# Performance work log

Measured on AMD Instinct MI355X. Metric: run time of the kernel, lower is better.

The kernel has to match this reference:

```python
import jax, jax.numpy as jnp
import numpy as np

LMAX = 3                               # self.lmax = lmax_arg(2) + 1
L2 = LMAX * LMAX                       # 9 = 1 + 3 + 5
N_MLP = 2
DEG_IDX = np.repeat(np.arange(LMAX), 2 * np.arange(LMAX) + 1)   # [9] block -> degree index
SEG = np.zeros((LMAX, L2), np.float32)                          # one-hot segment matrix [3,9]
SEG[DEG_IDX, np.arange(L2)] = 1.0


def setup_inputs() -> dict:
    key = jax.random.key(0)
    ks = jax.random.split(key, 8)
    B, M, F, K = 8, 1024, 64, 64
    x = jax.random.normal(ks[0], (B, M, F, L2), jnp.float32)
    y = jax.random.normal(ks[1], (B, M, F, L2), jnp.float32)
    # Glorot-ish scales so tanh stays in its active range
    s0 = 1.0 / np.sqrt(F * F * LMAX)
    sh = 1.0 / np.sqrt(K)
    wx0 = jax.random.normal(ks[2], (K, F, F, LMAX), jnp.float32) * s0
    wy0 = jax.random.normal(ks[3], (K, F, F, LMAX), jnp.float32) * s0
    wx_h = jax.random.normal(ks[4], (N_MLP, K, K), jnp.float32) * sh
    wy_h = jax.random.normal(ks[5], (N_MLP, K, K), jnp.float32) * sh
    wxf = jax.random.normal(ks[6], (LMAX, F, K), jnp.float32) * sh
    wyf = jax.random.normal(ks[7], (LMAX, F, K), jnp.float32) * sh
    return {"x": x, "y": y, "wx0": wx0, "wy0": wy0,
            "wx_h": wx_h, "wy_h": wy_h, "wxf": wxf, "wyf": wyf}


def reference(x, y, wx0, wy0, wx_h, wy_h, wxf, wyf):
    seg = jnp.asarray(SEG)                                   # [lmax, l2]
    # cross-product gate from the l=1 (vector) components
    x1 = x[..., 1:4]                                         # [B,M,F,3]
    y1 = y[..., 1:4]
    gate = jnp.sum(jnp.cross(x1, y1) * y[..., 0:3], axis=-1) # [B,M,F]
    xg = x * gate[..., None]                                 # gated x, [B,M,F,l2]
    # outer product over features + contiguous segment-sum over degree blocks
    # mix[b,m,f,g,l] = sum_{s in block l} xg[b,m,g,s] * y[b,m,f,s]
    mix = jnp.einsum('bmgs,bmfs,ls->bmfgl', xg, y, seg)      # [B,M,F,F,lmax]
    mix_x = jnp.einsum('bmfgl,kfgl->bmk', mix, wx0)          # [B,M,k]
    mix_y = jnp.einsum('bmfgl,kfgl->bmk', mix, wy0)
    for i in range(N_MLP):
        mix_x = jnp.tanh(mix_x @ wx_h[i])
        mix_y = jnp.tanh(mix_y @ wy_h[i])
    mix_x = jnp.tanh(jnp.einsum('bmk,lfk->bmfl', mix_x, wxf))  # [B,M,F,lmax]
    mix_y = jnp.tanh(jnp.einsum('bmk,lfk->bmfl', mix_y, wyf))
    # broadcast each degree back over its 2l+1 components (gather == tf.repeat)
    res = mix_x[..., DEG_IDX] * xg + mix_y[..., DEG_IDX] * y   # [B,M,F,l2]
    return res
```

## Files before the change

### kernel.cpp

```cpp
#include <hip/hip_runtime.h>
#include <hip/hip_bf16.h>

typedef __attribute__((ext_vector_type(8))) short short8;
typedef __attribute__((ext_vector_type(16))) float f32x16;
typedef __fp16 h2 __attribute__((ext_vector_type(2)));
typedef unsigned short ushort_t;

#define DEVFN static __device__ __forceinline__
#define MFMA32 __builtin_amdgcn_mfma_f32_32x32x16_bf16

DEVFN float bf2f(unsigned short u){
  union { unsigned int i; float f; } v; v.i = ((unsigned int)u) << 16; return v.f;
}
DEVFN unsigned short f2bf(float f){
  unsigned int u = __float_as_uint(f);
  unsigned int r = u + 0x7FFFu + ((u >> 16) & 1u);
  return (unsigned short)(r >> 16);
}
DEVFN unsigned int pkbf(float lo, float hi){
  __hip_bfloat162 h = __float22bfloat162_rn(make_float2(lo, hi));
  return *reinterpret_cast<unsigned int*>(&h);
}
DEVFN h2 pkrtz(float a, float b){ return __builtin_amdgcn_cvt_pkrtz(a, b); }
DEVFN h2 u2h(unsigned int u){ union { unsigned int u; h2 h; } v; v.u = u; return v.h; }
#if __has_builtin(__builtin_amdgcn_fdot2)
DEVFN float fdot2(h2 a, h2 b, float c){ return __builtin_amdgcn_fdot2(a, b, c, false); }
#else
DEVFN float fdot2(h2 a, h2 b, float c){ return c + (float)a[0]*(float)b[0] + (float)a[1]*(float)b[1]; }
#endif
DEVFN float tanh_fast(float x){
  float t = __builtin_amdgcn_exp2f(x * 2.885390081777926815f);
  return 1.0f - 2.0f * __builtin_amdgcn_rcpf(t + 1.0f);
}
DEVFN int kmap(int h, int j){ return 4*h + (j & 3) + 8*(j >> 2); }

__global__ void bake_w0(const float* __restrict__ wx0, const float* __restrict__ wy0,
                        ushort_t* __restrict__ wfrag){
  int slot = blockIdx.x * 256 + threadIdx.x;
  int lane = slot & 63;
  int q = slot >> 6;
  int blk = q % 6; int q2 = q / 6;
  int l = blk >> 1, nt = blk & 1;
  int nh = q2 & 1; int gq = (q2 >> 1) & 3; int f = q2 >> 3;
  int h = lane >> 5;
  int k = nt*32 + (lane & 31);
  const float* w = nh ? wy0 : wx0;
  unsigned int pk[4];
#pragma unroll
  for (int jj = 0; jj < 4; ++jj){
    int g0 = gq*16 + kmap(h, 2*jj);
    int g1 = gq*16 + kmap(h, 2*jj + 1);
    unsigned int b0 = f2bf(w[((k*64 + f)*64 + g0)*3 + l]);
    unsigned int b1 = f2bf(w[((k*64 + f)*64 + g1)*3 + l]);
    pk[jj] = b0 | (b1 << 16);
  }
  *reinterpret_cast<uint4*>(wfrag + (size_t)slot * 8) = make_uint4(pk[0], pk[1], pk[2], pk[3]);
}

__global__ void bake_wh(const float* __restrict__ wxh, const float* __restrict__ wyh,
                        ushort_t* __restrict__ whfrag){
  int slot = blockIdx.x * 256 + threadIdx.x;
  int lane = slot & 63;
  int q = slot >> 6;
  int nt = q & 1; q >>= 1;
  int c  = q & 3; q >>= 2;
  int path = q & 1; int layer = q >> 1;
  const float* w = path ? wyh : wxh;
  int n = nt*32 + (lane & 31);
  int h = lane >> 5;
  unsigned int pk[4];
#pragma unroll
  for (int jj = 0; jj < 4; ++jj){
    int k0 = c*16 + kmap(h, 2*jj);
    int k1 = c*16 + kmap(h, 2*jj + 1);
    unsigned int b0 = f2bf(w[layer*4096 + k0*64 + n]);
    unsigned int b1 = f2bf(w[layer*4096 + k1*64 + n]);
    pk[jj] = b0 | (b1 << 16);
  }
  *reinterpret_cast<uint4*>(whfrag + (size_t)slot * 8) = make_uint4(pk[0], pk[1], pk[2], pk[3]);
}

__global__ void bake_wf(const float* __restrict__ wxf, const float* __restrict__ wyf,
                        ushort_t* __restrict__ wffrag){
  int slot = blockIdx.x * 256 + threadIdx.x;
  int lane = slot & 63;
  int q = slot >> 6;
  int ntf = q % 6;
  int q2 = q / 6;
  int c = q2 & 3; int path = q2 >> 2;
  const float* w = path ? wyf : wxf;
  int n = ntf*32 + (lane & 31);
  int lw = n >> 6, fw = n & 63;
  int h = lane >> 5;
  unsigned int pk[4];
#pragma unroll
  for (int jj = 0; jj < 4; ++jj){
    int k0 = c*16 + kmap(h, 2*jj);
    int k1 = c*16 + kmap(h, 2*jj + 1);
    unsigned int b0 = f2bf(w[(lw*64 + fw)*64 + k0]);
    unsigned int b1 = f2bf(w[(lw*64 + fw)*64 + k1]);
    pk[jj] = b0 | (b1 << 16);
  }
  *reinterpret_cast<uint4*>(wffrag + (size_t)slot * 8) = make_uint4(pk[0], pk[1], pk[2], pk[3]);
}

struct BSet { uint4 b[6]; };
union U4 { uint4 u; short8 s; };

__global__ __launch_bounds__(256)
void gemm9(const float* __restrict__ x, const float* __restrict__ y,
           const ushort_t* __restrict__ wfrag, float* __restrict__ mix){
  extern __shared__ char lds[];
  unsigned int* YHd = (unsigned int*)lds;
  ushort_t* YHh = (ushort_t*)lds;
  float* Xf = (float*)(lds + 41600);
  float (*red)[64][33] = (float (*)[64][33])(lds + 41600);

  const int bid = blockIdx.x;
  const int id = (bid & 7)*64 + (bid >> 3);
  const int nh = id & 1, mb = id >> 1;
  const int pbase = mb * 32;

  const int t = threadIdx.x, lane = t & 63, gq = t >> 6;
  const int h = lane >> 5, pr = lane & 31;

  const float* xb = x + (size_t)pbase * 576;
  const float* yb = y + (size_t)pbase * 576;

#pragma unroll
  for (int c = 0; c < 18; ++c){
    int q = t + c*256;
    int p = q / 144, off = (q - p*144) * 4;
    float4 v = *(const float4*)(yb + p*576 + off);
#pragma unroll
    for (int i = 0; i < 4; ++i){
      int flat = off + i;
      int f = flat / 9, s = flat - f*9;
      float vv = (i==0) ? v.x : (i==1) ? v.y : (i==2) ? v.z : v.w;
      union { __fp16 hf; ushort_t u; } cv; cv.hf = (__fp16)vv;
      YHh[p*650 + f*10 + s] = cv.u;
    }
  }
#pragma unroll
  for (int c = 0; c < 9; ++c){
    int q = t + c*256;
    int p = q / 72, off = (q - p*72) * 4;
    float4 v = *(const float4*)(xb + p*576 + off);
    float* dst = Xf + p*290 + off;
    dst[0] = v.x; dst[1] = v.y; dst[2] = v.z; dst[3] = v.w;
  }
  __syncthreads();

  h2 xg[8][5];
  auto compute_xg = [&](int hf){
#pragma unroll
    for (int j = 0; j < 8; ++j){
      int gl = (gq & 1)*16 + kmap(h, j);
      int gg = hf*32 + gl;
      const float* xp = Xf + pr*290 + gl*9;
      unsigned int yd0 = YHd[pr*325 + gg*5 + 0];
      unsigned int yd1 = YHd[pr*325 + gg*5 + 1];
      h2 y01 = u2h(yd0), y23v = u2h(yd1);
      float y0 = (float)y01[0], y1 = (float)y01[1];
      float y2 = (float)y23v[0], y3 = (float)y23v[1];
      float x1 = xp[1], x2 = xp[2], x3 = xp[3];
      float gate = (x2*y3 - x3*y2)*y0 + (x3*y1 - x1*y3)*y1 + (x1*y2 - x2*y1)*y2;
      xg[j][0] = pkrtz(xp[0]*gate, x1*gate);
      xg[j][1] = pkrtz(x2*gate, x3*gate);
      xg[j][2] = pkrtz(xp[4]*gate, xp[5]*gate);
      xg[j][3] = pkrtz(xp[6]*gate, xp[7]*gate);
      xg[j][4] = pkrtz(xp[8]*gate, 0.f);
    }
  };
  if (gq < 2) compute_xg(0);
  __syncthreads();
#pragma unroll
  for (int c = 0; c < 9; ++c){
    int q = t + c*256;
    int p = q / 72, off = (q - p*72) * 4;
    float4 v = *(const float4*)(xb + p*576 + 288 + off);
    float* dst = Xf + p*290 + off;
    dst[0] = v.x; dst[1] = v.y; dst[2] = v.z; dst[3] = v.w;
  }
  __syncthreads();
  if (gq >= 2) compute_xg(1);
  __syncthreads();

  f32x16 acc0, acc1;
#pragma unroll
  for (int e = 0; e < 16; ++e){ acc0[e] = 0.f; acc1[e] = 0.f; }

  const ushort_t* wt = wfrag + (size_t)(gq*2 + nh)*3072 + (size_t)lane*8;
  const unsigned int* yrow = YHd + pr*325;

  auto ldB = [&](int f, BSet& B){
    const ushort_t* p0 = wt + (size_t)f * 24576;
#pragma unroll
    for (int i = 0; i < 6; ++i) B.b[i] = *reinterpret_cast<const uint4*>(p0 + i*512);
  };
  auto ldYh = [&](int f, unsigned int* Yr){
#pragma unroll
    for (int d = 0; d < 5; ++d) Yr[d] = yrow[f*5 + d];
  };
  auto agen_mfma = [&](const unsigned int* Yr, const BSet& B){
    h2 y0m = u2h(Yr[0] & 0xFFFFu);
    h2 y1m = u2h(Yr[0] & 0xFFFF0000u);
    h2 y23 = u2h(Yr[1]), y45 = u2h(Yr[2]), y67 = u2h(Yr[3]);
    h2 y8p = u2h(Yr[4] & 0xFFFFu);
    float a0[8], a1[8], a2[8];
#pragma unroll
    for (int j = 0; j < 8; ++j){
      a0[j] = fdot2(xg[j][0], y0m, 0.f);
      a1[j] = fdot2(xg[j][1], y23, fdot2(xg[j][0], y1m, 0.f));
      a2[j] = fdot2(xg[j][4], y8p, fdot2(xg[j][3], y67, fdot2(xg[j][2], y45, 0.f)));
    }
    U4 fA0, fA1, fA2;
    fA0.u = make_uint4(pkbf(a0[0],a0[1]), pkbf(a0[2],a0[3]), pkbf(a0[4],a0[5]), pkbf(a0[6],a0[7]));
    fA1.u = make_uint4(pkbf(a1[0],a1[1]), pkbf(a1[2],a1[3]), pkbf(a1[4],a1[5]), pkbf(a1[6],a1[7]));
    fA2.u = make_uint4(pkbf(a2[0],a2[1]), pkbf(a2[2],a2[3]), pkbf(a2[4],a2[5]), pkbf(a2[6],a2[7]));
    U4 b0, b1, b2, b3, b4, b5;
    b0.u = B.b[0]; b1.u = B.b[1]; b2.u = B.b[2];
    b3.u = B.b[3]; b4.u = B.b[4]; b5.u = B.b[5];
    acc0 = MFMA32(fA0.s, b0.s, acc0, 0, 0, 0);
    acc1 = MFMA32(fA0.s, b1.s, acc1, 0, 0, 0);
    acc0 = MFMA32(fA1.s, b2.s, acc0, 0, 0, 0);
    acc1 = MFMA32(fA1.s, b3.s, acc1, 0, 0, 0);
    acc0 = MFMA32(fA2.s, b4.s, acc0, 0, 0, 0);
    acc1 = MFMA32(fA2.s, b5.s, acc1, 0, 0, 0);
  };

  BSet Ba, Bb;
  unsigned int Ya[5], Yb[5];
  ldB(0, Ba); ldYh(0, Ya);
  ldB(1, Bb); ldYh(1, Yb);

#pragma unroll 1
  for (int s = 0; s < 64; s += 2){
    agen_mfma(Ya, Ba);
    const int s2 = (s + 2 < 64) ? s + 2 : 63;
    ldB(s2, Ba); ldYh(s2, Ya);
    agen_mfma(Yb, Bb);
    const int s3 = (s + 3 < 64) ? s + 3 : 63;
    ldB(s3, Bb); ldYh(s3, Yb);
  }

  __syncthreads();
  if (gq >= 2){
#pragma unroll
    for (int e = 0; e < 16; ++e){
      red[gq-2][lane][e]      = acc0[e];
      red[gq-2][lane][16 + e] = acc1[e];
    }
  }
  __syncthreads();
  if (gq < 2){
#pragma unroll
    for (int e = 0; e < 16; ++e){
      acc0[e] += red[gq][lane][e];
      acc1[e] += red[gq][lane][16 + e];
    }
  }
  __syncthreads();
  if (gq == 1){
#pragma unroll
    for (int e = 0; e < 16; ++e){
      red[0][lane][e]      = acc0[e];
      red[0][lane][16 + e] = acc1[e];
    }
  }
  __syncthreads();
  if (gq == 0){
#pragma unroll
    for (int e = 0; e < 16; ++e){
      float v0 = acc0[e] + red[0][lane][e];
      float v1 = acc1[e] + red[0][lane][16 + e];
      int rowm = (e & 3) + 8*(e >> 2) + 4*h;
      float* d = mix + (size_t)(pbase + rowm)*128 + nh*64 + pr;
      d[0]  = v0;
      d[32] = v1;
    }
  }
}

__global__ __launch_bounds__(256, 1)
void mlp_final(const float* __restrict__ x, const float* __restrict__ y,
               const ushort_t* __restrict__ whfrag,
               const ushort_t* __restrict__ wffrag,
               const float* __restrict__ mix, float* __restrict__ out){
  extern __shared__ char ldsm[];
  ushort_t* hw = (ushort_t*)ldsm;
  const int t = threadIdx.x;
  const long pbase = (long)blockIdx.x * 32;

  {
    int p = t >> 3, n0 = (t & 7) * 16;
    const float* src = mix + (pbase + p)*128 + n0;
    int path = n0 >> 6, nn = n0 & 63;
    ushort_t* dst = hw + (path*2)*2176 + p*68 + nn;
#pragma unroll
    for (int q2 = 0; q2 < 16; ++q2) dst[q2] = f2bf(src[q2]);
  }
  __syncthreads();

  const int w = t >> 6, lane = t & 63;
  const int path = w >> 1, ntw = w & 1;
  const int prow = lane & 31, h = lane >> 5;
  int cur = 0;

#pragma unroll
  for (int layer = 0; layer < 2; ++layer){
    const ushort_t* act = hw + (path*2 + cur)*2176;
    f32x16 acc;
#pragma unroll
    for (int r = 0; r < 16; ++r) acc[r] = 0.f;
#pragma unroll
    for (int c = 0; c < 4; ++c){
      int ab = prow*68 + c*16 + 4*h;
      ushort4 lo = *(const ushort4*)&act[ab];
      ushort4 hi = *(const ushort4*)&act[ab + 8];
      short8 av; av[0]=lo.x; av[1]=lo.y; av[2]=lo.z; av[3]=lo.w;
      av[4]=hi.x; av[5]=hi.y; av[6]=hi.z; av[7]=hi.w;
      short8 bv = *(const short8*)(whfrag + ((((layer*2 + path)*4 + c)*2 + ntw)*512 + lane*8));
      acc = MFMA32(av, bv, acc, 0, 0, 0);
    }
    ushort_t* nact = hw + (path*2 + (cur ^ 1))*2176;
#pragma unroll
    for (int r = 0; r < 16; ++r){
      int p = (r & 3) + 8*(r >> 2) + 4*h;
      nact[p*68 + ntw*32 + prow] = f2bf(tanh_fast(acc[r]));
    }
    cur ^= 1;
    __syncthreads();
  }

  {
    const ushort_t* act = hw + (path*2 + cur)*2176;
    ushort_t* ob = hw + 8704 + path*6272;
#pragma unroll
    for (int e = 0; e < 3; ++e){
      int ntf = ntw*3 + e;
      f32x16 acc;
#pragma unroll
      for (int r = 0; r < 16; ++r) acc[r] = 0.f;
#pragma unroll
      for (int c = 0; c < 4; ++c){
        int ab = prow*68 + c*16 + 4*h;
        ushort4 lo = *(const ushort4*)&act[ab];
        ushort4 hi = *(const ushort4*)&act[ab + 8];
        short8 av; av[0]=lo.x; av[1]=lo.y; av[2]=lo.z; av[3]=lo.w;
        av[4]=hi.x; av[5]=hi.y; av[6]=hi.z; av[7]=hi.w;
        short8 bv = *(const short8*)(wffrag + (((path*4 + c)*6 + ntf)*512 + lane*8));
        acc = MFMA32(av, bv, acc, 0, 0, 0);
      }
#pragma unroll
      for (int r = 0; r < 16; ++r){
        int p = (r & 3) + 8*(r >> 2) + 4*h;
        ob[p*196 + ntf*32 + prow] = f2bf(tanh_fast(acc[r]));
      }
    }
  }
  __syncthreads();

  const ushort_t* oxb = hw + 8704;
  const ushort_t* oyb = hw + 8704 + 6272;
#pragma unroll 1
  for (int rep = 0; rep < 8; ++rep){
    int idx = t + rep*256;
    int p = idx >> 6, fq = idx & 63;
    const float* xr = x + ((pbase + p)*64 + fq)*9;
    const float* yr = y + ((pbase + p)*64 + fq)*9;
    float xv[9], yv[9];
#pragma unroll
    for (int s = 0; s < 9; ++s){ xv[s] = xr[s]; yv[s] = yr[s]; }
    float c0 = xv[2]*yv[3] - xv[3]*yv[2];
    float c1 = xv[3]*yv[1] - xv[1]*yv[3];
    float c2 = xv[1]*yv[2] - xv[2]*yv[1];
    float gate = c0*yv[0] + c1*yv[1] + c2*yv[2];
    float ox0 = bf2f(oxb[p*196 + fq]);
    float ox1 = bf2f(oxb[p*196 + 64 + fq]);
    float ox2 = bf2f(oxb[p*196 + 128 + fq]);
    float oy0 = bf2f(oyb[p*196 + fq]);
    float oy1 = bf2f(oyb[p*196 + 64 + fq]);
    float oy2 = bf2f(oyb[p*196 + 128 + fq]);
    float* orow = out + ((pbase + p)*64 + fq)*9;
    orow[0] = ox0*xv[0]*gate + oy0*yv[0];
#pragma unroll
    for (int s = 1; s < 4; ++s) orow[s] = ox1*xv[s]*gate + oy1*yv[s];
#pragma unroll
    for (int s = 4; s < 9; ++s) orow[s] = ox2*xv[s]*gate + oy2*yv[s];
  }
}

extern "C" void kernel_launch(void* const* d_in, const int* in_sizes, int n_in,
                              void* d_out, int out_size, void* d_ws, size_t ws_size,
                              hipStream_t stream){
  (void)in_sizes; (void)n_in; (void)out_size; (void)ws_size;
  const float* x   = (const float*)d_in[0];
  const float* y   = (const float*)d_in[1];
  const float* wx0 = (const float*)d_in[2];
  const float* wy0 = (const float*)d_in[3];
  const float* wxh = (const float*)d_in[4];
  const float* wyh = (const float*)d_in[5];
  const float* wxf = (const float*)d_in[6];
  const float* wyf = (const float*)d_in[7];
  float* out = (float*)d_out;
  char* ws = (char*)d_ws;
  ushort_t* wfrag  = (ushort_t*)(ws);
  ushort_t* whfrag = (ushort_t*)(ws + 3145728);
  ushort_t* wffrag = (ushort_t*)(ws + 3178496);
  float* mix       = (float*)(ws + 3227648);

  (void)hipFuncSetAttribute((const void*)gemm9,
        hipFuncAttributeMaxDynamicSharedMemorySize, 78720);
  (void)hipFuncSetAttribute((const void*)mlp_final,
        hipFuncAttributeMaxDynamicSharedMemorySize, 43520);

  hipLaunchKernelGGL(bake_w0, dim3(768), dim3(256), 0, stream, wx0, wy0, wfrag);
  hipLaunchKernelGGL(bake_wh, dim3(8),   dim3(256), 0, stream, wxh, wyh, whfrag);
  hipLaunchKernelGGL(bake_wf, dim3(12),  dim3(256), 0, stream, wxf, wyf, wffrag);
  hipLaunchKernelGGL(gemm9,   dim3(512), dim3(256), 78720, stream, x, y, wfrag, mix);
  hipLaunchKernelGGL(mlp_final, dim3(256), dim3(256), 42496, stream, x, y, whfrag, wffrag, mix, out);
}
```

Baseline: 91.70 us.

## Read x directly from global in gemm, shrink LDS, coalesce w0 bake reads

The gemm kernel stops staging x in shared memory. Each warp now computes its gated-x fragments straight from global memory, with no two-phase staged compute. The cross-warp reduction becomes a serial 3-step accumulate into one small buffer, which cuts LDS from about 78KB to about 50KB per block so more blocks can be resident. The w0 bake kernel is rewritten to read weights contiguously (one thread per weight triple) and scatter 2-byte writes, and pkbf now uses an inline bf16 pack instruction. The cost is uncoalesced strided global reads of x and extra barriers in the reduction.

```diff
diff --git a/kernel.cpp b/kernel.cpp
--- a/kernel.cpp
+++ b/kernel.cpp
@@ -17,9 +17,10 @@
   unsigned int r = u + 0x7FFFu + ((u >> 16) & 1u);
   return (unsigned short)(r >> 16);
 }
-DEVFN unsigned int pkbf(float lo, float hi){
-  __hip_bfloat162 h = __float22bfloat162_rn(make_float2(lo, hi));
-  return *reinterpret_cast<unsigned int*>(&h);
+DEVFN unsigned int pkbf(float a, float b){
+  unsigned int r;
+  asm("v_cvt_pk_bf16_f32 %0, %1, %2" : "=v"(r) : "v"(a), "v"(b));
+  return r;
 }
 DEVFN h2 pkrtz(float a, float b){ return __builtin_amdgcn_cvt_pkrtz(a, b); }
 DEVFN h2 u2h(unsigned int u){ union { unsigned int u; h2 h; } v; v.u = u; return v.h; }
@@ -36,25 +37,22 @@
 
 __global__ void bake_w0(const float* __restrict__ wx0, const float* __restrict__ wy0,
                         ushort_t* __restrict__ wfrag){
-  int slot = blockIdx.x * 256 + threadIdx.x;
-  int lane = slot & 63;
-  int q = slot >> 6;
-  int blk = q % 6; int q2 = q / 6;
-  int l = blk >> 1, nt = blk & 1;
-  int nh = q2 & 1; int gq = (q2 >> 1) & 3; int f = q2 >> 3;
-  int h = lane >> 5;
-  int k = nt*32 + (lane & 31);
-  const float* w = nh ? wy0 : wx0;
-  unsigned int pk[4];
-#pragma unroll
-  for (int jj = 0; jj < 4; ++jj){
-    int g0 = gq*16 + kmap(h, 2*jj);
-    int g1 = gq*16 + kmap(h, 2*jj + 1);
-    unsigned int b0 = f2bf(w[((k*64 + f)*64 + g0)*3 + l]);
-    unsigned int b1 = f2bf(w[((k*64 + f)*64 + g1)*3 + l]);
-    pk[jj] = b0 | (b1 << 16);
-  }
-  *reinterpret_cast<uint4*>(wfrag + (size_t)slot * 8) = make_uint4(pk[0], pk[1], pk[2], pk[3]);
+  int idx = blockIdx.x * 256 + threadIdx.x;
+  int g = idx & 63; int r = idx >> 6;
+  int f = r & 63; r >>= 6;
+  int k = r & 63; int path = r >> 6;
+  const float* w = path ? wy0 : wx0;
+  const float* src = w + ((size_t)(k*64 + f)*64 + g)*3;
+  float v0 = src[0], v1 = src[1], v2 = src[2];
+  int gq = g >> 4, gl = g & 15;
+  int h = (gl >> 2) & 1;
+  int j = (gl & 3) | ((gl >> 3) << 2);
+  int lane = h*32 + (k & 31);
+  int nt = k >> 5;
+  size_t base = (size_t)((f*4 + gq)*2 + path)*3072 + (size_t)lane*8 + j;
+  wfrag[base + 0*512 + (size_t)nt*512] = f2bf(v0);
+  wfrag[base + 2*512 + (size_t)nt*512] = f2bf(v1);
+  wfrag[base + 4*512 + (size_t)nt*512] = f2bf(v2);
 }
 
 __global__ void bake_wh(const float* __restrict__ wxh, const float* __restrict__ wyh,
@@ -108,13 +106,12 @@
 union U4 { uint4 u; short8 s; };
 
 __global__ __launch_bounds__(256)
-void gemm9(const float* __restrict__ x, const float* __restrict__ y,
-           const ushort_t* __restrict__ wfrag, float* __restrict__ mix){
+void gemm10(const float* __restrict__ x, const float* __restrict__ y,
+            const ushort_t* __restrict__ wfrag, float* __restrict__ mix){
   extern __shared__ char lds[];
   unsigned int* YHd = (unsigned int*)lds;
   ushort_t* YHh = (ushort_t*)lds;
-  float* Xf = (float*)(lds + 41600);
-  float (*red)[64][33] = (float (*)[64][33])(lds + 41600);
+  float (*red)[33] = (float (*)[33])(lds + 41600);
 
   const int bid = blockIdx.x;
   const int id = (bid & 7)*64 + (bid >> 3);
@@ -124,7 +121,6 @@
   const int t = threadIdx.x, lane = t & 63, gq = t >> 6;
   const int h = lane >> 5, pr = lane & 31;
 
-  const float* xb = x + (size_t)pbase * 576;
   const float* yb = y + (size_t)pbase * 576;
 
 #pragma unroll
@@ -141,50 +137,26 @@
       YHh[p*650 + f*10 + s] = cv.u;
     }
   }
-#pragma unroll
-  for (int c = 0; c < 9; ++c){
-    int q = t + c*256;
-    int p = q / 72, off = (q - p*72) * 4;
-    float4 v = *(const float4*)(xb + p*576 + off);
-    float* dst = Xf + p*290 + off;
-    dst[0] = v.x; dst[1] = v.y; dst[2] = v.z; dst[3] = v.w;
-  }
   __syncthreads();
 
   h2 xg[8][5];
-  auto compute_xg = [&](int hf){
-#pragma unroll
-    for (int j = 0; j < 8; ++j){
-      int gl = (gq & 1)*16 + kmap(h, j);
-      int gg = hf*32 + gl;
-      const float* xp = Xf + pr*290 + gl*9;
-      unsigned int yd0 = YHd[pr*325 + gg*5 + 0];
-      unsigned int yd1 = YHd[pr*325 + gg*5 + 1];
-      h2 y01 = u2h(yd0), y23v = u2h(yd1);
-      float y0 = (float)y01[0], y1 = (float)y01[1];
-      float y2 = (float)y23v[0], y3 = (float)y23v[1];
-      float x1 = xp[1], x2 = xp[2], x3 = xp[3];
-      float gate = (x2*y3 - x3*y2)*y0 + (x3*y1 - x1*y3)*y1 + (x1*y2 - x2*y1)*y2;
-      xg[j][0] = pkrtz(xp[0]*gate, x1*gate);
-      xg[j][1] = pkrtz(x2*gate, x3*gate);
-      xg[j][2] = pkrtz(xp[4]*gate, xp[5]*gate);
-      xg[j][3] = pkrtz(xp[6]*gate, xp[7]*gate);
-      xg[j][4] = pkrtz(xp[8]*gate, 0.f);
-    }
-  };
-  if (gq < 2) compute_xg(0);
-  __syncthreads();
-#pragma unroll
-  for (int c = 0; c < 9; ++c){
-    int q = t + c*256;
-    int p = q / 72, off = (q - p*72) * 4;
-    float4 v = *(const float4*)(xb + p*576 + 288 + off);
-    float* dst = Xf + p*290 + off;
-    dst[0] = v.x; dst[1] = v.y; dst[2] = v.z; dst[3] = v.w;
-  }
-  __syncthreads();
-  if (gq >= 2) compute_xg(1);
-  __syncthreads();
+#pragma unroll
+  for (int j = 0; j < 8; ++j){
+    const int g = gq*16 + kmap(h, j);
+    const float* xp = x + (size_t)(pbase + pr)*576 + g*9;
+    unsigned int yd0 = YHd[pr*325 + g*5 + 0];
+    unsigned int yd1 = YHd[pr*325 + g*5 + 1];
+    h2 y01 = u2h(yd0), y23v = u2h(yd1);
+    float y0 = (float)y01[0], y1 = (float)y01[1];
+    float y2 = (float)y23v[0], y3 = (float)y23v[1];
+    float x1 = xp[1], x2 = xp[2], x3 = xp[3];
+    float gate = (x2*y3 - x3*y2)*y0 + (x3*y1 - x1*y3)*y1 + (x1*y2 - x2*y1)*y2;
+    xg[j][0] = pkrtz(xp[0]*gate, x1*gate);
+    xg[j][1] = pkrtz(x2*gate, x3*gate);
+    xg[j][2] = pkrtz(xp[4]*gate, xp[5]*gate);
+    xg[j][3] = pkrtz(xp[6]*gate, xp[7]*gate);
+    xg[j][4] = pkrtz(xp[8]*gate, 0.f);
+  }
 
   f32x16 acc0, acc1;
 #pragma unroll
@@ -245,39 +217,32 @@
   }
 
   __syncthreads();
-  if (gq >= 2){
+#pragma unroll 1
+  for (int rr = 1; rr <= 3; ++rr){
+    if (gq == rr){
+#pragma unroll
+      for (int e = 0; e < 16; ++e){
+        red[lane][e]      = acc0[e];
+        red[lane][16 + e] = acc1[e];
+      }
+    }
+    __syncthreads();
+    if (gq == 0){
+#pragma unroll
+      for (int e = 0; e < 16; ++e){
+        acc0[e] += red[lane][e];
+        acc1[e] += red[lane][16 + e];
+      }
+    }
+    __syncthreads();
+  }
+  if (gq == 0){
 #pragma unroll
     for (int e = 0; e < 16; ++e){
-      red[gq-2][lane][e]      = acc0[e];
-      red[gq-2][lane][16 + e] = acc1[e];
-    }
-  }
-  __syncthreads();
-  if (gq < 2){
-#pragma unroll
-    for (int e = 0; e < 16; ++e){
-      acc0[e] += red[gq][lane][e];
-      acc1[e] += red[gq][lane][16 + e];
-    }
-  }
-  __syncthreads();
-  if (gq == 1){
-#pragma unroll
-    for (int e = 0; e < 16; ++e){
-      red[0][lane][e]      = acc0[e];
-      red[0][lane][16 + e] = acc1[e];
-    }
-  }
-  __syncthreads();
-  if (gq == 0){
-#pragma unroll
-    for (int e = 0; e < 16; ++e){
-      float v0 = acc0[e] + red[0][lane][e];
-      float v1 = acc1[e] + red[0][lane][16 + e];
       int rowm = (e & 3) + 8*(e >> 2) + 4*h;
       float* d = mix + (size_t)(pbase + rowm)*128 + nh*64 + pr;
-      d[0]  = v0;
-      d[32] = v1;
+      d[0]  = acc0[e];
+      d[32] = acc1[e];
     }
   }
 }
@@ -410,14 +375,14 @@
   ushort_t* wffrag = (ushort_t*)(ws + 3178496);
   float* mix       = (float*)(ws + 3227648);
 
-  (void)hipFuncSetAttribute((const void*)gemm9,
-        hipFuncAttributeMaxDynamicSharedMemorySize, 78720);
+  (void)hipFuncSetAttribute((const void*)gemm10,
+        hipFuncAttributeMaxDynamicSharedMemorySize, 50048);
   (void)hipFuncSetAttribute((const void*)mlp_final,
         hipFuncAttributeMaxDynamicSharedMemorySize, 43520);
 
-  hipLaunchKernelGGL(bake_w0, dim3(768), dim3(256), 0, stream, wx0, wy0, wfrag);
-  hipLaunchKernelGGL(bake_wh, dim3(8),   dim3(256), 0, stream, wxh, wyh, whfrag);
-  hipLaunchKernelGGL(bake_wf, dim3(12),  dim3(256), 0, stream, wxf, wyf, wffrag);
-  hipLaunchKernelGGL(gemm9,   dim3(512), dim3(256), 78720, stream, x, y, wfrag, mix);
+  hipLaunchKernelGGL(bake_w0, dim3(2048), dim3(256), 0, stream, wx0, wy0, wfrag);
+  hipLaunchKernelGGL(bake_wh, dim3(8),    dim3(256), 0, stream, wxh, wyh, whfrag);
+  hipLaunchKernelGGL(bake_wf, dim3(12),   dim3(256), 0, stream, wxf, wyf, wffrag);
+  hipLaunchKernelGGL(gemm10,  dim3(512),  dim3(256), 50048, stream, x, y, wfrag, mix);
   hipLaunchKernelGGL(mlp_final, dim3(256), dim3(256), 42496, stream, x, y, whfrag, wffrag, mix, out);
 }
```

After: 90.78 us. Within noise of the previous version (-1.0%).
